# Optimization experiments

Hardware: AMD Instinct MI355X
Metric: run time of the kernel (lower is better)

## Reference

```python
import jax, jax.numpy as jnp
import numpy as np

DIM = 3072
NUM_HEADS = 24
HEAD_DIM = 128
SEQ = 2048
BATCH = 1
EPS = 1e-6


def _make_rope(seq_len: int, head_dim: int):
    # Standard RoPE angles; cos/sin laid out per interleaved-pair convention
    # (each frequency repeated for the (real, imag) pair), shape [S, head_dim].
    half = head_dim // 2
    inv_freq = 1.0 / (10000.0 ** (np.arange(0, half, dtype=np.float32) / half))
    t = np.arange(seq_len, dtype=np.float32)
    freqs = np.outer(t, inv_freq)  # [S, half]
    freqs = np.repeat(freqs, 2, axis=-1)  # [S, head_dim], pairs share the angle
    return jnp.asarray(np.cos(freqs)), jnp.asarray(np.sin(freqs))


def setup_inputs() -> dict:
    key = jax.random.key(0)
    ks = jax.random.split(key, 8)
    inner = NUM_HEADS * HEAD_DIM
    s = 0.02
    hidden_states = jax.random.normal(ks[0], (BATCH, SEQ, DIM), dtype=jnp.float32)
    wq = jax.random.normal(ks[1], (inner, DIM), dtype=jnp.float32) * s
    wk = jax.random.normal(ks[2], (inner, DIM), dtype=jnp.float32) * s
    wv = jax.random.normal(ks[3], (inner, DIM), dtype=jnp.float32) * s
    bq = jax.random.normal(ks[4], (inner,), dtype=jnp.float32) * s
    bk = jax.random.normal(ks[5], (inner,), dtype=jnp.float32) * s
    bv = jax.random.normal(ks[6], (inner,), dtype=jnp.float32) * s
    norm_q_w = jnp.ones((HEAD_DIM,), dtype=jnp.float32)
    norm_k_w = jnp.ones((HEAD_DIM,), dtype=jnp.float32)
    cos, sin = _make_rope(SEQ, HEAD_DIM)
    return {
        "hidden_states": hidden_states,
        "wq": wq, "bq": bq, "wk": wk, "bk": bk, "wv": wv, "bv": bv,
        "norm_q_w": norm_q_w, "norm_k_w": norm_k_w,
        "cos": cos, "sin": sin,
    }


def _rms_norm(x, w, eps=EPS):
    # RMSNorm over the last (head_dim) axis.
    var = jnp.mean(jnp.square(x), axis=-1, keepdims=True)
    return x * jax.lax.rsqrt(var + eps) * w


def _apply_rope(x, cos, sin):
    # x: [B, S, H, D]; cos/sin: [S, D]. Interleaved-pair rotation
    # (diffusers apply_rotary_emb, use_real_unbind_dim=-1).
    xr = x[..., 0::2]
    xi = x[..., 1::2]
    rot = jnp.stack([-xi, xr], axis=-1).reshape(x.shape)
    c = cos[None, :, None, :]
    s = sin[None, :, None, :]
    return x * c + rot * s


def reference(hidden_states, wq, bq, wk, bk, wv, bv, norm_q_w, norm_k_w, cos, sin):
    B, S, _ = hidden_states.shape
    H, D = NUM_HEADS, HEAD_DIM
    # QKV projections (ColumnParallelLinear with tp_size=1)
    q = (hidden_states @ wq.T + bq).reshape(B, S, H, D)
    k = (hidden_states @ wk.T + bk).reshape(B, S, H, D)
    v = (hidden_states @ wv.T + bv).reshape(B, S, H, D)
    # qk-norm then RoPE
    q = _apply_rope(_rms_norm(q, norm_q_w), cos, sin)
    k = _apply_rope(_rms_norm(k, norm_k_w), cos, sin)
    # Non-causal full attention
    scale = 1.0 / jnp.sqrt(jnp.asarray(D, dtype=q.dtype))
    scores = jnp.einsum("bqhd,bkhd->bhqk", q, k) * scale
    probs = jax.nn.softmax(scores, axis=-1)
    out = jnp.einsum("bhqk,bkhd->bqhd", probs, v)
    return out.reshape(B, S, H * D).astype(q.dtype)
```

## Files before the change

### kernel.cpp

```cpp
#include <hip/hip_runtime.h>

#define S_LEN 2048
#define DIMSZ 3072
#define NHEAD 24
#define HDIM 128
#define NQKV 9216
#define QSCALE 0.08838834764831845f
#define FMAX 12.0f

typedef unsigned short u16;
typedef unsigned int u32;
typedef __attribute__((ext_vector_type(8))) short short8;
typedef __attribute__((ext_vector_type(4))) float f32x4;

__device__ __forceinline__ u16 f2bf(float f) {
    u32 u = __float_as_uint(f);
    u32 r = (u + 0x7fffu + ((u >> 16) & 1u)) >> 16;
    return (u16)r;
}
__device__ __forceinline__ float bf2f(u16 u) {
    return __uint_as_float((u32)u << 16);
}
__device__ __forceinline__ u32 cvtpk_bf16(float lo, float hi) {
    u32 r;
    asm("v_cvt_pk_bf16_f32 %0, %1, %2" : "=v"(r) : "v"(lo), "v"(hi));
    return r;
}

__device__ __forceinline__ void lds16(u16* lds, const u16* g) {
    __builtin_amdgcn_global_load_lds((const __attribute__((address_space(1))) u32*)g,
                                     (__attribute__((address_space(3))) u32*)lds, 16, 0, 0);
}

__global__ void k_conv(const float4* __restrict__ hs, const float4* __restrict__ wq,
                       const float4* __restrict__ wk, const float4* __restrict__ wv,
                       u16* __restrict__ hs_b, u16* __restrict__ w_b) {
    for (int i = blockIdx.x * 256 + threadIdx.x; i < 8650752; i += 2048 * 256) {
        const float4* src;
        u16* dst;
        if (i < 1572864) { src = hs + i; dst = hs_b + (size_t)i * 4; }
        else if (i < 3932160) { src = wq + (i - 1572864); dst = w_b + (size_t)(i - 1572864) * 4; }
        else if (i < 6291456) { src = wk + (i - 3932160); dst = w_b + 9437184 + (size_t)(i - 3932160) * 4; }
        else { src = wv + (i - 6291456); dst = w_b + 18874368 + (size_t)(i - 6291456) * 4; }
        float4 v = *src;
        u32 lo = (u32)f2bf(v.x) | ((u32)f2bf(v.y) << 16);
        u32 hi = (u32)f2bf(v.z) | ((u32)f2bf(v.w) << 16);
        uint2 p; p.x = lo; p.y = hi;
        *(uint2*)dst = p;
    }
}

__global__ __launch_bounds__(256, 2) void k_gemm(const u16* __restrict__ A, const u16* __restrict__ W,
                                                 u16* __restrict__ C) {
    __shared__ __align__(16) u16 As[2][256 * 32];
    __shared__ __align__(16) u16 Bs[2][192 * 32];
    const int tid = threadIdx.x, wave = tid >> 6, lane = tid & 63;
    const int bm = blockIdx.x & 7, bn = blockIdx.x >> 3;
    const int frow = lane & 15, fk = lane >> 4;
    const u16* baseA = A + (size_t)(bm * 256) * DIMSZ;

    auto stageA = [&](int b, int kt) {
#pragma unroll
        for (int j = 0; j < 4; ++j) {
            int flat = j * 256 + tid, row = flat >> 2, ch = flat & 3;
            lds16(&As[b][flat * 8], baseA + (size_t)row * DIMSZ + kt * 32 + ((ch ^ ((row >> 1) & 3)) * 8));
        }
    };
    auto stageB = [&](int b, int kt) {
#pragma unroll
        for (int j = 0; j < 3; ++j) {
            int flat = j * 256 + tid, row = flat >> 2, ch = flat & 3;
            int srow = bn * 144 + row;
            srow = (srow > NQKV - 1) ? (NQKV - 1) : srow;
            lds16(&Bs[b][flat * 8], W + (size_t)srow * DIMSZ + kt * 32 + ((ch ^ ((row >> 1) & 3)) * 8));
        }
    };

    stageA(0, 0); stageB(0, 0); stageA(1, 1); stageB(1, 1);
    asm volatile("s_waitcnt vmcnt(7)");
    __builtin_amdgcn_s_barrier();

    f32x4 acc[4][9] = {};
    for (int T = 0; T < 96; ++T) {
        const int b = T & 1;
        const u16* LA = As[b];
        const u16* LB = Bs[b];
        short8 af[4], bf[9];
#pragma unroll
        for (int mf = 0; mf < 4; ++mf) {
            int row = wave * 64 + mf * 16 + frow;
            af[mf] = *(const short8*)&LA[row * 32 + ((fk ^ ((row >> 1) & 3)) * 8)];
        }
#pragma unroll
        for (int nf = 0; nf < 9; ++nf) {
            int row = nf * 16 + frow;
            bf[nf] = *(const short8*)&LB[row * 32 + ((fk ^ ((row >> 1) & 3)) * 8)];
        }
        __builtin_amdgcn_s_setprio(1);
#pragma unroll
        for (int mf = 0; mf < 4; ++mf)
#pragma unroll
            for (int nf = 0; nf < 9; ++nf)
                acc[mf][nf] = __builtin_amdgcn_mfma_f32_16x16x32_bf16(af[mf], bf[nf], acc[mf][nf], 0, 0, 0);
        __builtin_amdgcn_s_setprio(0);
        __builtin_amdgcn_s_barrier();
        if (T < 94) {
            stageA(b, T + 2); stageB(b, T + 2);
            asm volatile("s_waitcnt vmcnt(7)");
            __builtin_amdgcn_s_barrier();
        } else if (T == 94) {
            asm volatile("s_waitcnt vmcnt(0)");
            __builtin_amdgcn_s_barrier();
        }
    }

#pragma unroll
    for (int mf = 0; mf < 4; ++mf) {
#pragma unroll
        for (int nf = 0; nf < 9; ++nf) {
            int n = bn * 144 + nf * 16 + frow;
#pragma unroll
            for (int i = 0; i < 4; ++i) {
                int m = bm * 256 + wave * 64 + mf * 16 + fk * 4 + i;
                C[(size_t)m * NQKV + n] = f2bf(acc[mf][nf][i]);
            }
        }
    }
}

__global__ void k_post(const u16* __restrict__ qkv, const float* __restrict__ nw_q,
                       const float* __restrict__ nw_k, const float* __restrict__ bq,
                       const float* __restrict__ bk, const float* __restrict__ bv,
                       const float* __restrict__ cosT, const float* __restrict__ sinT,
                       u16* __restrict__ Qb, u16* __restrict__ Kb, u16* __restrict__ Vt) {
    const int tid = threadIdx.x;
    const int row = blockIdx.x * 16 + (tid >> 4);
    const int lane16 = tid & 15;
    const int s = row & 2047, h = row >> 11;
    const int d0 = lane16 * 8;
    const u16* base = qkv + (size_t)s * NQKV + h * HDIM + d0;

    float cs[8], sn[8];
    *(float4*)&cs[0] = *(const float4*)&cosT[s * HDIM + d0];
    *(float4*)&cs[4] = *(const float4*)&cosT[s * HDIM + d0 + 4];
    *(float4*)&sn[0] = *(const float4*)&sinT[s * HDIM + d0];
    *(float4*)&sn[4] = *(const float4*)&sinT[s * HDIM + d0 + 4];

    {
        short8 raw = *(const short8*)base;
        float b[8];
        *(float4*)&b[0] = *(const float4*)&bq[h * HDIM + d0];
        *(float4*)&b[4] = *(const float4*)&bq[h * HDIM + d0 + 4];
        float x[8], ss = 0.f;
#pragma unroll
        for (int j = 0; j < 8; ++j) { x[j] = bf2f((u16)raw[j]) + b[j]; ss += x[j] * x[j]; }
#pragma unroll
        for (int m = 1; m < 16; m <<= 1) ss += __shfl_xor(ss, m);
        float r = rsqrtf(ss * (1.0f / 128.0f) + 1e-6f);
        float w[8];
        *(float4*)&w[0] = *(const float4*)&nw_q[d0];
        *(float4*)&w[4] = *(const float4*)&nw_q[d0 + 4];
        u32 pk[4];
#pragma unroll
        for (int jp = 0; jp < 4; ++jp) {
            float e = x[2 * jp] * r * w[2 * jp];
            float o = x[2 * jp + 1] * r * w[2 * jp + 1];
            float y0 = (e * cs[2 * jp] - o * sn[2 * jp]) * QSCALE;
            float y1 = (o * cs[2 * jp] + e * sn[2 * jp]) * QSCALE;
            pk[jp] = cvtpk_bf16(y0, y1);
        }
        uint4 v; v.x = pk[0]; v.y = pk[1]; v.z = pk[2]; v.w = pk[3];
        *(uint4*)&Qb[((size_t)h * S_LEN + s) * HDIM + d0] = v;
    }
    {
        short8 raw = *(const short8*)(base + 3072);
        float b[8];
        *(float4*)&b[0] = *(const float4*)&bk[h * HDIM + d0];
        *(float4*)&b[4] = *(const float4*)&bk[h * HDIM + d0 + 4];
        float x[8], ss = 0.f;
#pragma unroll
        for (int j = 0; j < 8; ++j) { x[j] = bf2f((u16)raw[j]) + b[j]; ss += x[j] * x[j]; }
#pragma unroll
        for (int m = 1; m < 16; m <<= 1) ss += __shfl_xor(ss, m);
        float r = rsqrtf(ss * (1.0f / 128.0f) + 1e-6f);
        float w[8];
        *(float4*)&w[0] = *(const float4*)&nw_k[d0];
        *(float4*)&w[4] = *(const float4*)&nw_k[d0 + 4];
        u32 pk[4];
#pragma unroll
        for (int jp = 0; jp < 4; ++jp) {
            float e = x[2 * jp] * r * w[2 * jp];
            float o = x[2 * jp + 1] * r * w[2 * jp + 1];
            float y0 = e * cs[2 * jp] - o * sn[2 * jp];
            float y1 = o * cs[2 * jp] + e * sn[2 * jp];
            pk[jp] = cvtpk_bf16(y0, y1);
        }
        uint4 v; v.x = pk[0]; v.y = pk[1]; v.z = pk[2]; v.w = pk[3];
        *(uint4*)&Kb[((size_t)h * S_LEN + s) * HDIM + d0] = v;
    }
    {
        short8 raw = *(const short8*)(base + 6144);
        float b[8];
        *(float4*)&b[0] = *(const float4*)&bv[h * HDIM + d0];
        *(float4*)&b[4] = *(const float4*)&bv[h * HDIM + d0 + 4];
#pragma unroll
        for (int j = 0; j < 8; ++j)
            Vt[((size_t)h * HDIM + d0 + j) * S_LEN + s] = f2bf(bf2f((u16)raw[j]) + b[j]);
    }
}

__global__ __launch_bounds__(128, 2) void k_attn(const u16* __restrict__ Qb, const u16* __restrict__ Kb,
                                                 const u16* __restrict__ Vt, float* __restrict__ out) {
    __shared__ __align__(16) u16 Ks[2][32 * 128];
    __shared__ __align__(16) u16 Vs[2][128 * 32];
    __shared__ __align__(16) u16 Ps[2][32 * 32];
    const int tid = threadIdx.x;
    const int wave = tid >> 6, lane = tid & 63;
    const int wg = (blockIdx.x & 7) * 96 + (blockIdx.x >> 3);
    const int h = wg >> 5, qb = wg & 31;
    const int frow = lane & 15, fk = lane >> 4;

    short8 qf[2][4];
#pragma unroll
    for (int qg = 0; qg < 2; ++qg) {
        const u16* qbase = Qb + ((size_t)h * S_LEN + qb * 64 + wave * 32 + qg * 16 + frow) * HDIM + fk * 8;
#pragma unroll
        for (int ks = 0; ks < 4; ++ks) qf[qg][ks] = *(const short8*)(qbase + ks * 32);
    }

    f32x4 o[2][8] = {};
    float l_p[2] = {0.f, 0.f};

#define STAGE(buf, kt)                                                                        \
    {                                                                                         \
        _Pragma("unroll") for (int c = 0; c < 4; ++c) {                                       \
            int flat = c * 128 + tid;                                                         \
            int r = flat >> 4, ch = flat & 15;                                                \
            lds16(Ks[buf] + flat * 8,                                                         \
                  Kb + ((size_t)h * S_LEN + (kt) * 32 + r) * HDIM + ((ch ^ (r & 15)) * 8));   \
        }                                                                                     \
        _Pragma("unroll") for (int c = 0; c < 4; ++c) {                                       \
            int flat = c * 128 + tid;                                                         \
            int r = flat >> 2, ch = flat & 3;                                                 \
            lds16(Vs[buf] + flat * 8,                                                         \
                  Vt + ((size_t)h * HDIM + r) * S_LEN + (kt) * 32 + ((ch ^ ((r >> 2) & 3)) * 8)); \
        }                                                                                     \
    }

    STAGE(0, 0);
    __syncthreads();
    int cur = 0;

    for (int kt = 0; kt < 64; ++kt) {
        if (kt + 1 < 64) STAGE(cur ^ 1, kt + 1);
        f32x4 sacc[2][2] = {};
        __builtin_amdgcn_s_setprio(1);
#pragma unroll
        for (int nf = 0; nf < 2; ++nf) {
#pragma unroll
            for (int ks = 0; ks < 4; ++ks) {
                short8 kf = *(const short8*)&Ks[cur][(nf * 16 + frow) * 128 + (((ks * 4 + fk) ^ frow) * 8)];
#pragma unroll
                for (int qg = 0; qg < 2; ++qg)
                    sacc[qg][nf] = __builtin_amdgcn_mfma_f32_16x16x32_bf16(kf, qf[qg][ks], sacc[qg][nf], 0, 0, 0);
            }
        }
        __builtin_amdgcn_s_setprio(0);
#pragma unroll
        for (int qg = 0; qg < 2; ++qg) {
            int prow = qg * 16 + frow;
#pragma unroll
            for (int nf = 0; nf < 2; ++nf) {
                float p0 = __expf(sacc[qg][nf][0] - FMAX);
                float p1 = __expf(sacc[qg][nf][1] - FMAX);
                float p2 = __expf(sacc[qg][nf][2] - FMAX);
                float p3 = __expf(sacc[qg][nf][3] - FMAX);
                l_p[qg] += (p0 + p1) + (p2 + p3);
                uint2 pk;
                pk.x = cvtpk_bf16(p0, p1);
                pk.y = cvtpk_bf16(p2, p3);
                int c16 = (nf * 2 + (fk >> 1)) ^ ((prow >> 2) & 3);
                *(uint2*)&Ps[wave][prow * 32 + c16 * 8 + (fk & 1) * 4] = pk;
            }
        }
        short8 pf[2];
#pragma unroll
        for (int qg = 0; qg < 2; ++qg)
            pf[qg] = *(const short8*)&Ps[wave][(qg * 16 + frow) * 32 + ((fk ^ ((frow >> 2) & 3)) * 8)];
        __builtin_amdgcn_s_setprio(1);
#pragma unroll
        for (int nf8 = 0; nf8 < 8; ++nf8) {
            short8 vf = *(const short8*)&Vs[cur][(nf8 * 16 + frow) * 32 + ((fk ^ ((frow >> 2) & 3)) * 8)];
#pragma unroll
            for (int qg = 0; qg < 2; ++qg)
                o[qg][nf8] = __builtin_amdgcn_mfma_f32_16x16x32_bf16(pf[qg], vf, o[qg][nf8], 0, 0, 0);
        }
        __builtin_amdgcn_s_setprio(0);
        __syncthreads();
        cur ^= 1;
    }
#undef STAGE

#pragma unroll
    for (int qg = 0; qg < 2; ++qg) {
        l_p[qg] += __shfl_xor(l_p[qg], 16);
        l_p[qg] += __shfl_xor(l_p[qg], 32);
    }

#pragma unroll
    for (int qg = 0; qg < 2; ++qg)
#pragma unroll
        for (int i = 0; i < 4; ++i) {
            float rinv = 1.0f / __shfl(l_p[qg], fk * 4 + i);
            int srow = qb * 64 + wave * 32 + qg * 16 + fk * 4 + i;
#pragma unroll
            for (int nf8 = 0; nf8 < 8; ++nf8)
                out[(size_t)srow * DIMSZ + h * HDIM + nf8 * 16 + frow] = o[qg][nf8][i] * rinv;
        }
}

extern "C" void kernel_launch(void* const* d_in, const int* in_sizes, int n_in,
                              void* d_out, int out_size, void* d_ws, size_t ws_size,
                              hipStream_t stream) {
    const float* hs = (const float*)d_in[0];
    const float* wq = (const float*)d_in[1];
    const float* bq = (const float*)d_in[2];
    const float* wk = (const float*)d_in[3];
    const float* bk = (const float*)d_in[4];
    const float* wv = (const float*)d_in[5];
    const float* bv = (const float*)d_in[6];
    const float* nq = (const float*)d_in[7];
    const float* nk = (const float*)d_in[8];
    const float* cosT = (const float*)d_in[9];
    const float* sinT = (const float*)d_in[10];
    float* out = (float*)d_out;

    char* ws = (char*)d_ws;
    u16* hs_b = (u16*)(ws);
    u16* w_b = (u16*)(ws + 12582912);
    u16* qkv = (u16*)(ws + 69206016);
    u16* Qb = (u16*)(ws + 106954752);
    u16* Kb = (u16*)(ws + 119537664);
    u16* Vt = (u16*)(ws + 132120576);

    k_conv<<<dim3(2048), 256, 0, stream>>>((const float4*)hs, (const float4*)wq,
                                           (const float4*)wk, (const float4*)wv, hs_b, w_b);

    k_gemm<<<dim3(512), 256, 0, stream>>>(hs_b, w_b, qkv);

    k_post<<<dim3(3072), 256, 0, stream>>>(qkv, nq, nk, bq, bk, bv, cosT, sinT, Qb, Kb, Vt);

    k_attn<<<dim3(768), 128, 0, stream>>>(Qb, Kb, Vt, out);
}
```

Before: 283.0 us.

## Software-pipeline attention so PV of previous tile overlaps QK of current

Restructures the attention loop so that the P·V MFMA for tile kt-1 is issued after the QK^T and softmax of tile kt. This lets the exp work and the matrix work of adjacent tiles interleave. To support this, V gets a triple-buffered LDS slot and P a double-buffered per-wave slot, with a drain step after the loop. It also adds memory clobbers to the inline waitcnt asm in the GEMM so the compiler cannot reorder loads across them. The cost is extra LDS use and more complex buffer indexing, which could affect occupancy.

```diff
diff --git a/kernel.cpp b/kernel.cpp
--- a/kernel.cpp
+++ b/kernel.cpp
@@ -77,7 +77,7 @@
     };
 
     stageA(0, 0); stageB(0, 0); stageA(1, 1); stageB(1, 1);
-    asm volatile("s_waitcnt vmcnt(7)");
+    asm volatile("s_waitcnt vmcnt(7)" ::: "memory");
     __builtin_amdgcn_s_barrier();
 
     f32x4 acc[4][9] = {};
@@ -106,10 +106,10 @@
         __builtin_amdgcn_s_barrier();
         if (T < 94) {
             stageA(b, T + 2); stageB(b, T + 2);
-            asm volatile("s_waitcnt vmcnt(7)");
+            asm volatile("s_waitcnt vmcnt(7)" ::: "memory");
             __builtin_amdgcn_s_barrier();
         } else if (T == 94) {
-            asm volatile("s_waitcnt vmcnt(0)");
+            asm volatile("s_waitcnt vmcnt(0)" ::: "memory");
             __builtin_amdgcn_s_barrier();
         }
     }
@@ -212,8 +212,8 @@
 __global__ __launch_bounds__(128, 2) void k_attn(const u16* __restrict__ Qb, const u16* __restrict__ Kb,
                                                  const u16* __restrict__ Vt, float* __restrict__ out) {
     __shared__ __align__(16) u16 Ks[2][32 * 128];
-    __shared__ __align__(16) u16 Vs[2][128 * 32];
-    __shared__ __align__(16) u16 Ps[2][32 * 32];
+    __shared__ __align__(16) u16 Vs[3][128 * 32];
+    __shared__ __align__(16) u16 Ps[2][2][32 * 32];
     const int tid = threadIdx.x;
     const int wave = tid >> 6, lane = tid & 63;
     const int wg = (blockIdx.x & 7) * 96 + (blockIdx.x >> 3);
@@ -231,41 +231,48 @@
     f32x4 o[2][8] = {};
     float l_p[2] = {0.f, 0.f};
 
-#define STAGE(buf, kt)                                                                        \
+#define STAGE_K(slot, kt)                                                                     \
     {                                                                                         \
         _Pragma("unroll") for (int c = 0; c < 4; ++c) {                                       \
             int flat = c * 128 + tid;                                                         \
             int r = flat >> 4, ch = flat & 15;                                                \
-            lds16(Ks[buf] + flat * 8,                                                         \
+            lds16(Ks[slot] + flat * 8,                                                        \
                   Kb + ((size_t)h * S_LEN + (kt) * 32 + r) * HDIM + ((ch ^ (r & 15)) * 8));   \
         }                                                                                     \
+    }
+#define STAGE_V(slot, kt)                                                                     \
+    {                                                                                         \
         _Pragma("unroll") for (int c = 0; c < 4; ++c) {                                       \
             int flat = c * 128 + tid;                                                         \
             int r = flat >> 2, ch = flat & 3;                                                 \
-            lds16(Vs[buf] + flat * 8,                                                         \
+            lds16(Vs[slot] + flat * 8,                                                        \
                   Vt + ((size_t)h * HDIM + r) * S_LEN + (kt) * 32 + ((ch ^ ((r >> 2) & 3)) * 8)); \
         }                                                                                     \
     }
 
-    STAGE(0, 0);
+    STAGE_K(0, 0); STAGE_V(0, 0);
     __syncthreads();
-    int cur = 0;
 
     for (int kt = 0; kt < 64; ++kt) {
-        if (kt + 1 < 64) STAGE(cur ^ 1, kt + 1);
+        if (kt + 1 < 64) {
+            STAGE_K((kt + 1) & 1, kt + 1);
+            STAGE_V((kt + 1) % 3, kt + 1);
+        }
+        const u16* LK = Ks[kt & 1];
         f32x4 sacc[2][2] = {};
         __builtin_amdgcn_s_setprio(1);
 #pragma unroll
         for (int nf = 0; nf < 2; ++nf) {
 #pragma unroll
             for (int ks = 0; ks < 4; ++ks) {
-                short8 kf = *(const short8*)&Ks[cur][(nf * 16 + frow) * 128 + (((ks * 4 + fk) ^ frow) * 8)];
+                short8 kf = *(const short8*)&LK[(nf * 16 + frow) * 128 + (((ks * 4 + fk) ^ frow) * 8)];
 #pragma unroll
                 for (int qg = 0; qg < 2; ++qg)
                     sacc[qg][nf] = __builtin_amdgcn_mfma_f32_16x16x32_bf16(kf, qf[qg][ks], sacc[qg][nf], 0, 0, 0);
             }
         }
         __builtin_amdgcn_s_setprio(0);
+        u16* PW = Ps[wave][kt & 1];
 #pragma unroll
         for (int qg = 0; qg < 2; ++qg) {
             int prow = qg * 16 + frow;
@@ -280,26 +287,45 @@
                 pk.x = cvtpk_bf16(p0, p1);
                 pk.y = cvtpk_bf16(p2, p3);
                 int c16 = (nf * 2 + (fk >> 1)) ^ ((prow >> 2) & 3);
-                *(uint2*)&Ps[wave][prow * 32 + c16 * 8 + (fk & 1) * 4] = pk;
+                *(uint2*)&PW[prow * 32 + c16 * 8 + (fk & 1) * 4] = pk;
             }
         }
+        if (kt > 0) {
+            const u16* LV = Vs[(kt - 1) % 3];
+            const u16* PR = Ps[wave][(kt - 1) & 1];
+            short8 pf[2];
+#pragma unroll
+            for (int qg = 0; qg < 2; ++qg)
+                pf[qg] = *(const short8*)&PR[(qg * 16 + frow) * 32 + ((fk ^ ((frow >> 2) & 3)) * 8)];
+            __builtin_amdgcn_s_setprio(1);
+#pragma unroll
+            for (int nf8 = 0; nf8 < 8; ++nf8) {
+                short8 vf = *(const short8*)&LV[(nf8 * 16 + frow) * 32 + ((fk ^ ((frow >> 2) & 3)) * 8)];
+#pragma unroll
+                for (int qg = 0; qg < 2; ++qg)
+                    o[qg][nf8] = __builtin_amdgcn_mfma_f32_16x16x32_bf16(pf[qg], vf, o[qg][nf8], 0, 0, 0);
+            }
+            __builtin_amdgcn_s_setprio(0);
+        }
+        __syncthreads();
+    }
+    {
+        const u16* LV = Vs[0];
+        const u16* PR = Ps[wave][1];
         short8 pf[2];
 #pragma unroll
         for (int qg = 0; qg < 2; ++qg)
-            pf[qg] = *(const short8*)&Ps[wave][(qg * 16 + frow) * 32 + ((fk ^ ((frow >> 2) & 3)) * 8)];
-        __builtin_amdgcn_s_setprio(1);
+            pf[qg] = *(const short8*)&PR[(qg * 16 + frow) * 32 + ((fk ^ ((frow >> 2) & 3)) * 8)];
 #pragma unroll
         for (int nf8 = 0; nf8 < 8; ++nf8) {
-            short8 vf = *(const short8*)&Vs[cur][(nf8 * 16 + frow) * 32 + ((fk ^ ((frow >> 2) & 3)) * 8)];
+            short8 vf = *(const short8*)&LV[(nf8 * 16 + frow) * 32 + ((fk ^ ((frow >> 2) & 3)) * 8)];
 #pragma unroll
             for (int qg = 0; qg < 2; ++qg)
                 o[qg][nf8] = __builtin_amdgcn_mfma_f32_16x16x32_bf16(pf[qg], vf, o[qg][nf8], 0, 0, 0);
         }
-        __builtin_amdgcn_s_setprio(0);
-        __syncthreads();
-        cur ^= 1;
-    }
-#undef STAGE
+    }
+#undef STAGE_K
+#undef STAGE_V
 
 #pragma unroll
     for (int qg = 0; qg < 2; ++qg) {
```

Result: no change. 285.7 us (+0.9%).
